# Kernel tuning notes

Measured on AMD Instinct MI355X. Metric: run time of the kernel, lower is better.

Reference implementation:

```python
import jax, jax.numpy as jnp
import numpy as np

B, N, DIN, D, NH, NL = 4, 256, 4, 64, 4, 2
DH = D // NH
EPS = 1e-5
SLOPE = 0.01  # torch LeakyReLU default negative_slope


def setup_inputs() -> dict:
    key = jax.random.key(0)
    ks = jax.random.split(key, 16)
    def p(k, shape, s=0.05):
        return jax.random.normal(k, shape, jnp.float32) * s
    return {
        "feature": jax.random.normal(ks[0], (B, N, N, DIN), jnp.float32),
        "W1": p(ks[1], (DIN, D)), "b1": jnp.zeros((D,), jnp.float32),
        "mw": p(ks[2], (NH, D)), "mb": jnp.zeros((NH,), jnp.float32),
        "bn_gamma": jnp.ones((D,), jnp.float32), "bn_beta": jnp.zeros((D,), jnp.float32),
        "Wq": p(ks[3], (NL, D, D)), "bq": jnp.zeros((NL, D), jnp.float32),
        "Wk": p(ks[4], (NL, D, D)), "bk": jnp.zeros((NL, D), jnp.float32),
        "Wv": p(ks[5], (NL, D, D)), "bv": jnp.zeros((NL, D), jnp.float32),
        "Wo": p(ks[6], (NL, D, D)), "bo": jnp.zeros((NL, D), jnp.float32),
        "ln1_g": jnp.ones((NL, D), jnp.float32), "ln1_b": jnp.zeros((NL, D), jnp.float32),
        "Wff1": p(ks[7], (NL, D, 2 * D)), "bff1": jnp.zeros((NL, 2 * D), jnp.float32),
        "Wff2": p(ks[8], (NL, 2 * D, D)), "bff2": jnp.zeros((NL, D), jnp.float32),
        "ln2_g": jnp.ones((NL, D), jnp.float32), "ln2_b": jnp.zeros((NL, D), jnp.float32),
    }


def _leaky(x):
    return jnp.where(x >= 0, x, SLOPE * x)


def _layer_norm(x, g, b):
    m = x.mean(axis=-1, keepdims=True)
    v = x.var(axis=-1, keepdims=True)
    return g * (x - m) / jnp.sqrt(v + EPS) + b


def reference(feature, W1, b1, mw, mb, bn_gamma, bn_beta,
              Wq, bq, Wk, bk, Wv, bv, Wo, bo, ln1_g, ln1_b,
              Wff1, bff1, Wff2, bff2, ln2_g, ln2_b):
    # linear1: (B,N,N,DIN) -> (B,N,N,D)
    feat = feature @ W1 + b1
    # per-head scalar attention score over node pairs: (NH,B,N,N)
    s = jnp.einsum('bijh,nh->nbij', feat, mw) + mb[:, None, None, None]
    w = jnp.exp(_leaky(s))
    w = w / w.sum(axis=3, keepdims=True)  # softmax-like over second node dim j
    # weighted aggregation: sum over i, then mean over heads -> (B,N,D)
    h = jnp.einsum('nbij,bijh->bjh', w, feat) / NH
    # BatchNorm1d over channels D, stats over (B,N) (training-mode, biased var)
    m = h.mean(axis=(0, 1))
    v = h.var(axis=(0, 1))
    x = bn_gamma * (h - m) / jnp.sqrt(v + EPS) + bn_beta  # (B,N,D)
    # standard post-LN TransformerEncoder, NL layers
    scale = 1.0 / np.sqrt(DH).astype(np.float32)
    for l in range(NL):
        q = (x @ Wq[l] + bq[l]).reshape(B, N, NH, DH)
        k = (x @ Wk[l] + bk[l]).reshape(B, N, NH, DH)
        vv = (x @ Wv[l] + bv[l]).reshape(B, N, NH, DH)
        a = jax.nn.softmax(jnp.einsum('bqhd,bkhd->bhqk', q, k) * scale, axis=-1)
        o = jnp.einsum('bhqk,bkhd->bqhd', a, vv).reshape(B, N, D) @ Wo[l] + bo[l]
        x = _layer_norm(x + o, ln1_g[l], ln1_b[l])
        f = jax.nn.relu(x @ Wff1[l] + bff1[l]) @ Wff2[l] + bff2[l]
        x = _layer_norm(x + f, ln2_g[l], ln2_b[l])
    return x
```

## Files before the change

kernel.cpp:

```cpp
#include <hip/hip_runtime.h>
#include <math.h>

#define B 4
#define N 256
#define DIN 4
#define D 64
#define NH 4
#define NL 2
#define DH 16

constexpr float EPS = 1e-5f;
constexpr float SLOPE = 0.01f;

__device__ __forceinline__ void mc_proj(
    const float* __restrict__ W1, const float* __restrict__ b1,
    const float* __restrict__ mw, const float* __restrict__ mb,
    int lane, float* Mreg , float* Creg ) {
    float w1v[4];
#pragma unroll
    for (int kk = 0; kk < 4; ++kk) w1v[kk] = W1[kk * D + lane];
    float b1v = b1[lane];
#pragma unroll
    for (int n = 0; n < 4; ++n) {
        float mwv = mw[n * D + lane];
        float p0 = w1v[0] * mwv, p1 = w1v[1] * mwv;
        float p2 = w1v[2] * mwv, p3 = w1v[3] * mwv;
        float pc = b1v * mwv;
#pragma unroll
        for (int off = 32; off > 0; off >>= 1) {
            p0 += __shfl_xor(p0, off); p1 += __shfl_xor(p1, off);
            p2 += __shfl_xor(p2, off); p3 += __shfl_xor(p3, off);
            pc += __shfl_xor(pc, off);
        }
        Mreg[n * 4 + 0] = p0; Mreg[n * 4 + 1] = p1;
        Mreg[n * 4 + 2] = p2; Mreg[n * 4 + 3] = p3;
        Creg[n] = pc + mb[n];
    }
}

__global__ void __launch_bounds__(512) k_rowsum(
    const float* __restrict__ feature, const float* __restrict__ W1,
    const float* __restrict__ b1, const float* __restrict__ mw,
    const float* __restrict__ mb, float* __restrict__ rs,
    float* __restrict__ bnacc ) {
    __shared__ float part[32];
    int t = threadIdx.x;
    int lane = t & 63, w = t >> 6;
    int cb = blockIdx.x;
    if (cb == 0 && t < 128) bnacc[t] = 0.f;

    int r = w & 3, mh = w >> 2;
    int bi = cb * 4 + r;
    const float4* fb = (const float4*)(feature) + (size_t)bi * N;
    float4 f0 = fb[lane + 64 * (mh * 2 + 0)];
    float4 f1 = fb[lane + 64 * (mh * 2 + 1)];

    float Mreg[16], Creg[4];
    mc_proj(W1, b1, mw, mb, lane, Mreg, Creg);

    float sn[4] = {0.f, 0.f, 0.f, 0.f};
#pragma unroll
    for (int mm = 0; mm < 2; ++mm) {
        float4 f = (mm == 0) ? f0 : f1;
#pragma unroll
        for (int n = 0; n < 4; ++n) {
            float s = Creg[n] + f.x * Mreg[n*4+0] + f.y * Mreg[n*4+1]
                              + f.z * Mreg[n*4+2] + f.w * Mreg[n*4+3];
            s = (s >= 0.f) ? s : SLOPE * s;
            sn[n] += __expf(s);
        }
    }
#pragma unroll
    for (int n = 0; n < 4; ++n)
#pragma unroll
        for (int off = 32; off > 0; off >>= 1) sn[n] += __shfl_xor(sn[n], off);
    if (lane == 0) {
#pragma unroll
        for (int n = 0; n < 4; ++n) part[w * 4 + n] = sn[n];
    }
    __syncthreads();
    if (t < 16) {
        int rr = t >> 2, n = t & 3;
        rs[((size_t)(cb * 4 + rr)) * 4 + n] = part[rr * 4 + n] + part[(rr + 4) * 4 + n];
    }
}

__global__ void __launch_bounds__(512) k_aggregate(
    const float* __restrict__ feature, const float* __restrict__ W1,
    const float* __restrict__ b1, const float* __restrict__ mw,
    const float* __restrict__ mb, const float* __restrict__ rs,
    float* __restrict__ h, float* __restrict__ bnacc) {
    __shared__ float part[8][10];
    __shared__ float gacc[20];
    __shared__ float hs[4][D];
    int t = threadIdx.x;
    int lane = t & 63, w = t >> 6;
    int cb = blockIdx.x;

    int b = cb >> 6, j0 = (cb & 63) * 4;
    int i = t & 255, jh = t >> 8;
    const float4* fb = (const float4*)(feature) + ((size_t)(b * N + i) * N + j0 + jh * 2);
    float4 f[2];
    f[0] = fb[0];
    f[1] = fb[1];
    float4 r4 = *(const float4*)(rs + (size_t)(b * N + i) * 4);

    float Mreg[16], Creg[4];
    mc_proj(W1, b1, mw, mb, lane, Mreg, Creg);
    float w1v[4];
#pragma unroll
    for (int kk = 0; kk < 4; ++kk) w1v[kk] = W1[kk * D + lane];
    float b1v = b1[lane];

    float rinv[4] = {1.f / r4.x, 1.f / r4.y, 1.f / r4.z, 1.f / r4.w};
    float acc[2][5];
#pragma unroll
    for (int jj = 0; jj < 2; ++jj) {
        float wbar = 0.f;
#pragma unroll
        for (int n = 0; n < 4; ++n) {
            float s = Creg[n] + f[jj].x * Mreg[n*4+0] + f[jj].y * Mreg[n*4+1]
                              + f[jj].z * Mreg[n*4+2] + f[jj].w * Mreg[n*4+3];
            s = (s >= 0.f) ? s : SLOPE * s;
            wbar += __expf(s) * rinv[n];
        }
        wbar *= 0.25f;
        acc[jj][0] = wbar * f[jj].x; acc[jj][1] = wbar * f[jj].y;
        acc[jj][2] = wbar * f[jj].z; acc[jj][3] = wbar * f[jj].w;
        acc[jj][4] = wbar;
    }
#pragma unroll
    for (int jj = 0; jj < 2; ++jj)
#pragma unroll
        for (int c = 0; c < 5; ++c)
#pragma unroll
            for (int off = 32; off > 0; off >>= 1) acc[jj][c] += __shfl_xor(acc[jj][c], off);
    if (lane == 0) {
#pragma unroll
        for (int jj = 0; jj < 2; ++jj)
#pragma unroll
            for (int c = 0; c < 5; ++c) part[w][jj * 5 + c] = acc[jj][c];
    }
    __syncthreads();
    if (t < 20) {
        int jj = t / 5, c = t - jj * 5;
        int g = jj >> 1, jjl = jj & 1;
        gacc[t] = part[g*4+0][jjl*5+c] + part[g*4+1][jjl*5+c]
                + part[g*4+2][jjl*5+c] + part[g*4+3][jjl*5+c];
    }
    __syncthreads();
    if (t < 256) {
        float hv = gacc[w * 5 + 4] * b1v;
#pragma unroll
        for (int kk = 0; kk < 4; ++kk) hv += gacc[w * 5 + kk] * w1v[kk];
        h[((size_t)(b * N + j0 + w)) * D + lane] = hv;
        hs[w][lane] = hv;
    }
    __syncthreads();
    if (t < 64) {
        float s = hs[0][lane] + hs[1][lane] + hs[2][lane] + hs[3][lane];
        float sq = hs[0][lane]*hs[0][lane] + hs[1][lane]*hs[1][lane]
                 + hs[2][lane]*hs[2][lane] + hs[3][lane]*hs[3][lane];
        atomicAdd(bnacc + lane, s);
        atomicAdd(bnacc + D + lane, sq);
    }
}

__global__ void __launch_bounds__(256, 2) k_qkv0(
    const float* __restrict__ h, const float* __restrict__ bnacc,
    const float* __restrict__ bn_g, const float* __restrict__ bn_b,
    const float* __restrict__ Wq, const float* __restrict__ bq,
    const float* __restrict__ Wk, const float* __restrict__ bk,
    const float* __restrict__ Wv, const float* __restrict__ bv,
    float* __restrict__ x, float* __restrict__ q,
    float* __restrict__ k, float* __restrict__ v) {
    __shared__ float xs[2][D];
    __shared__ float pp[4][2][192];
    int t = threadIdx.x, lane = t & 63, w = t >> 6, ch = lane;
    int b = blockIdx.x, n0 = blockIdx.y * 2;

    float wq[16], wk[16], wv[16];
#pragma unroll
    for (int i = 0; i < 16; ++i) {
        int kk = w * 16 + i;
        wq[i] = Wq[kk * D + ch];
        wk[i] = Wk[kk * D + ch];
        wv[i] = Wv[kk * D + ch];
    }
    float mean = bnacc[ch] * (1.0f / (B * N));
    float var = bnacc[D + ch] * (1.0f / (B * N)) - mean * mean;
    float inv = rsqrtf(var + EPS);
    size_t xi0 = ((size_t)(b * N + n0)) * D + ch;
    float xv0 = bn_g[ch] * (h[xi0] - mean) * inv + bn_b[ch];
    float xv1 = bn_g[ch] * (h[xi0 + D] - mean) * inv + bn_b[ch];
    if (w == 0) { x[xi0] = xv0; xs[0][ch] = xv0; }
    if (w == 1) { x[xi0 + D] = xv1; xs[1][ch] = xv1; }
    __syncthreads();

    float aq0=0.f, ak0=0.f, av0=0.f, aq1=0.f, ak1=0.f, av1=0.f;
#pragma unroll
    for (int i = 0; i < 16; ++i) {
        int kk = w * 16 + i;
        float xx0 = xs[0][kk], xx1 = xs[1][kk];
        aq0 += xx0 * wq[i]; ak0 += xx0 * wk[i]; av0 += xx0 * wv[i];
        aq1 += xx1 * wq[i]; ak1 += xx1 * wk[i]; av1 += xx1 * wv[i];
    }
    pp[w][0][ch] = aq0; pp[w][0][64 + ch] = ak0; pp[w][0][128 + ch] = av0;
    pp[w][1][ch] = aq1; pp[w][1][64 + ch] = ak1; pp[w][1][128 + ch] = av1;
    __syncthreads();
    if (w < 3) {
        int o = w * 64;
        int head = ch >> 4, dh = ch & (DH - 1);
#pragma unroll
        for (int tk = 0; tk < 2; ++tk) {
            float val = pp[0][tk][o+ch] + pp[1][tk][o+ch] + pp[2][tk][o+ch] + pp[3][tk][o+ch];
            size_t oidx = (((size_t)(b * NH + head)) * N + (n0 + tk)) * DH + dh;
            if (w == 0) q[oidx] = val + bq[ch];
            else if (w == 1) k[oidx] = val + bk[ch];
            else v[oidx] = val + bv[ch];
        }
    }
}

template <bool FUSE>
__global__ void __launch_bounds__(256, 2) k_layer(
    const float* __restrict__ q, const float* __restrict__ k,
    const float* __restrict__ v,
    const float* __restrict__ Wo, const float* __restrict__ bo,
    const float* __restrict__ ln1g, const float* __restrict__ ln1b,
    const float* __restrict__ Wff1, const float* __restrict__ bff1,
    const float* __restrict__ Wff2, const float* __restrict__ bff2,
    const float* __restrict__ ln2g, const float* __restrict__ ln2b,
    const float* __restrict__ Wqn, const float* __restrict__ bqn,
    const float* __restrict__ Wkn, const float* __restrict__ bkn,
    const float* __restrict__ Wvn, const float* __restrict__ bvn,
    float* __restrict__ qo, float* __restrict__ ko, float* __restrict__ vo,
    float* __restrict__ x) {
    __shared__ float attS[2][D];
    __shared__ float xs[2][D];
    __shared__ float f1s[2][2 * D];
    __shared__ float ppA[4][2][192];
    __shared__ float ppB[4][2][192];
    int t = threadIdx.x, lane = t & 63, w = t >> 6, ch = lane;
    int b = blockIdx.x, n0 = blockIdx.y * 2;

    size_t xi0 = ((size_t)(b * N + n0)) * D + ch;
    float xv0 = x[xi0], xv1 = x[xi0 + D];
    float bo_r = bo[ch], l1g = ln1g[ch], l1b = ln1b[ch];
    float bf1a = bff1[ch], bf1b = bff1[D + ch];
    float bf2_r = bff2[ch], l2g = ln2g[ch], l2b = ln2b[ch];

    int bh = b * NH + w;
    const float4* qp0 = (const float4*)(q + ((size_t)bh * N + n0) * DH);
    const float4* qp1 = (const float4*)(q + ((size_t)bh * N + n0 + 1) * DH);
    float4 qv0[4], qv1[4];
#pragma unroll
    for (int c = 0; c < 4; ++c) { qv0[c] = qp0[c]; qv1[c] = qp1[c]; }
    const float* kb = k + (size_t)bh * N * DH;
    const float* vb = v + (size_t)bh * N * DH;
    float o0[DH], o1[DH];
#pragma unroll
    for (int d = 0; d < DH; ++d) { o0[d] = 0.f; o1[d] = 0.f; }
    float l0 = 0.f, l1 = 0.f;
#pragma unroll 1
    for (int cc = 0; cc < 4; ++cc) {
        int key = cc * 64 + lane;
        const float4* kp4 = (const float4*)(kb + (size_t)key * DH);
        const float4* vp4 = (const float4*)(vb + (size_t)key * DH);
        float4 Kc[4], Vc[4];
#pragma unroll
        for (int c = 0; c < 4; ++c) { Kc[c] = kp4[c]; Vc[c] = vp4[c]; }
        float s0 = 0.f, s1 = 0.f;
#pragma unroll
        for (int c = 0; c < 4; ++c) {
            s0 += qv0[c].x * Kc[c].x + qv0[c].y * Kc[c].y +
                  qv0[c].z * Kc[c].z + qv0[c].w * Kc[c].w;
            s1 += qv1[c].x * Kc[c].x + qv1[c].y * Kc[c].y +
                  qv1[c].z * Kc[c].z + qv1[c].w * Kc[c].w;
        }
        float p0 = __expf(s0 * 0.25f);
        float p1 = __expf(s1 * 0.25f);
        l0 += p0; l1 += p1;
#pragma unroll
        for (int c = 0; c < 4; ++c) {
            o0[4*c+0] += p0 * Vc[c].x; o0[4*c+1] += p0 * Vc[c].y;
            o0[4*c+2] += p0 * Vc[c].z; o0[4*c+3] += p0 * Vc[c].w;
            o1[4*c+0] += p1 * Vc[c].x; o1[4*c+1] += p1 * Vc[c].y;
            o1[4*c+2] += p1 * Vc[c].z; o1[4*c+3] += p1 * Vc[c].w;
        }
    }
    float wo[16];
#pragma unroll
    for (int i = 0; i < 16; ++i) wo[i] = Wo[(w * 16 + i) * D + ch];

#pragma unroll
    for (int off = 32; off > 0; off >>= 1) {
        l0 += __shfl_xor(l0, off);
        l1 += __shfl_xor(l1, off);
    }
#pragma unroll
    for (int d = 0; d < DH; ++d) {
#pragma unroll
        for (int off = 32; off > 0; off >>= 1) {
            o0[d] += __shfl_xor(o0[d], off);
            o1[d] += __shfl_xor(o1[d], off);
        }
    }
    float rl0 = 1.f / l0, rl1 = 1.f / l1;
    if (lane < DH) {
        float sel0 = o0[0], sel1 = o1[0];
#pragma unroll
        for (int d = 1; d < DH; ++d)
            if (lane == d) { sel0 = o0[d]; sel1 = o1[d]; }
        attS[0][w * DH + lane] = sel0 * rl0;
        attS[1][w * DH + lane] = sel1 * rl1;
    }
    __syncthreads();

    {
        float a0 = 0.f, a1 = 0.f;
#pragma unroll
        for (int i = 0; i < 16; ++i) {
            int kk = w * 16 + i;
            float wv = wo[i];
            a0 += attS[0][kk] * wv;
            a1 += attS[1][kk] * wv;
        }
        ppA[w][0][ch] = a0; ppA[w][1][ch] = a1;
    }
    float wf1a[16], wf1b[16];
#pragma unroll
    for (int i = 0; i < 16; ++i) {
        int kk = w * 16 + i;
        wf1a[i] = Wff1[kk * 2 * D + ch];
        wf1b[i] = Wff1[kk * 2 * D + D + ch];
    }
    __syncthreads();

    float r0 = xv0 + bo_r + ppA[0][0][ch] + ppA[1][0][ch] + ppA[2][0][ch] + ppA[3][0][ch];
    float r1 = xv1 + bo_r + ppA[0][1][ch] + ppA[1][1][ch] + ppA[2][1][ch] + ppA[3][1][ch];
    float s0a = r0, q0a = r0 * r0, s1a = r1, q1a = r1 * r1;
#pragma unroll
    for (int off = 32; off > 0; off >>= 1) {
        s0a += __shfl_xor(s0a, off); q0a += __shfl_xor(q0a, off);
        s1a += __shfl_xor(s1a, off); q1a += __shfl_xor(q1a, off);
    }
    float mean10 = s0a * (1.0f / D), var10 = q0a * (1.0f / D) - mean10 * mean10;
    float mean11 = s1a * (1.0f / D), var11 = q1a * (1.0f / D) - mean11 * mean11;
    float x1_0 = l1g * (r0 - mean10) * rsqrtf(var10 + EPS) + l1b;
    float x1_1 = l1g * (r1 - mean11) * rsqrtf(var11 + EPS) + l1b;
    if (w == 0) xs[0][ch] = x1_0;
    if (w == 1) xs[1][ch] = x1_1;
    __syncthreads();

    {
        float u0=0.f, g0=0.f, u1=0.f, g1=0.f;
#pragma unroll
        for (int i = 0; i < 16; ++i) {
            int kk = w * 16 + i;
            float xx0 = xs[0][kk], xx1 = xs[1][kk];
            u0 += xx0 * wf1a[i]; g0 += xx0 * wf1b[i];
            u1 += xx1 * wf1a[i]; g1 += xx1 * wf1b[i];
        }
        ppB[w][0][ch] = u0; ppB[w][0][64 + ch] = g0;
        ppB[w][1][ch] = u1; ppB[w][1][64 + ch] = g1;
    }
    float wf2[32];
#pragma unroll
    for (int i = 0; i < 32; ++i) wf2[i] = Wff2[(w * 32 + i) * D + ch];
    __syncthreads();

    {
        float a00 = fmaxf(bf1a + ppB[0][0][ch] + ppB[1][0][ch] + ppB[2][0][ch] + ppB[3][0][ch], 0.f);
        float a01 = fmaxf(bf1b + ppB[0][0][64+ch] + ppB[1][0][64+ch] + ppB[2][0][64+ch] + ppB[3][0][64+ch], 0.f);
        float a10 = fmaxf(bf1a + ppB[0][1][ch] + ppB[1][1][ch] + ppB[2][1][ch] + ppB[3][1][ch], 0.f);
        float a11 = fmaxf(bf1b + ppB[0][1][64+ch] + ppB[1][1][64+ch] + ppB[2][1][64+ch] + ppB[3][1][64+ch], 0.f);
        if (w == 0) { f1s[0][ch] = a00; f1s[0][64 + ch] = a01; }
        if (w == 1) { f1s[1][ch] = a10; f1s[1][64 + ch] = a11; }
    }
    __syncthreads();

    {
        float e0 = 0.f, e1 = 0.f;
#pragma unroll
        for (int i = 0; i < 32; ++i) {
            int kk = w * 32 + i;
            float xx0 = f1s[0][kk], xx1 = f1s[1][kk];
            e0 += xx0 * wf2[i];
            e1 += xx1 * wf2[i];
        }
        ppA[w][0][ch] = e0; ppA[w][1][ch] = e1;
    }
    float wqn[16], wkn[16], wvn[16];
    if (FUSE) {
#pragma unroll
        for (int i = 0; i < 16; ++i) {
            int kk = w * 16 + i;
            wqn[i] = Wqn[kk * D + ch];
            wkn[i] = Wkn[kk * D + ch];
            wvn[i] = Wvn[kk * D + ch];
        }
    }
    __syncthreads();

    float o2_0 = bf2_r + ppA[0][0][ch] + ppA[1][0][ch] + ppA[2][0][ch] + ppA[3][0][ch];
    float o2_1 = bf2_r + ppA[0][1][ch] + ppA[1][1][ch] + ppA[2][1][ch] + ppA[3][1][ch];
    float r20 = x1_0 + o2_0, r21 = x1_1 + o2_1;
    float s0b = r20, q0b = r20 * r20, s1b = r21, q1b = r21 * r21;
#pragma unroll
    for (int off = 32; off > 0; off >>= 1) {
        s0b += __shfl_xor(s0b, off); q0b += __shfl_xor(q0b, off);
        s1b += __shfl_xor(s1b, off); q1b += __shfl_xor(q1b, off);
    }
    float mean20 = s0b * (1.0f / D), var20 = q0b * (1.0f / D) - mean20 * mean20;
    float mean21 = s1b * (1.0f / D), var21 = q1b * (1.0f / D) - mean21 * mean21;
    float xn0 = l2g * (r20 - mean20) * rsqrtf(var20 + EPS) + l2b;
    float xn1 = l2g * (r21 - mean21) * rsqrtf(var21 + EPS) + l2b;
    if (w == 0) x[xi0] = xn0;
    if (w == 1) x[xi0 + D] = xn1;

    if (FUSE) {
        if (w == 0) xs[0][ch] = xn0;
        if (w == 1) xs[1][ch] = xn1;
        __syncthreads();
        float aq0=0.f, ak0=0.f, av0=0.f, aq1=0.f, ak1=0.f, av1=0.f;
#pragma unroll
        for (int i = 0; i < 16; ++i) {
            int kk = w * 16 + i;
            float xx0 = xs[0][kk], xx1 = xs[1][kk];
            aq0 += xx0 * wqn[i]; ak0 += xx0 * wkn[i]; av0 += xx0 * wvn[i];
            aq1 += xx1 * wqn[i]; ak1 += xx1 * wkn[i]; av1 += xx1 * wvn[i];
        }
        ppB[w][0][ch] = aq0; ppB[w][0][64 + ch] = ak0; ppB[w][0][128 + ch] = av0;
        ppB[w][1][ch] = aq1; ppB[w][1][64 + ch] = ak1; ppB[w][1][128 + ch] = av1;
        __syncthreads();
        if (w < 3) {
            int o = w * 64;
            int head = ch >> 4, dh = ch & (DH - 1);
#pragma unroll
            for (int tk = 0; tk < 2; ++tk) {
                float val = ppB[0][tk][o+ch] + ppB[1][tk][o+ch] + ppB[2][tk][o+ch] + ppB[3][tk][o+ch];
                size_t oidx = (((size_t)(b * NH + head)) * N + (n0 + tk)) * DH + dh;
                if (w == 0) qo[oidx] = val + bqn[ch];
                else if (w == 1) ko[oidx] = val + bkn[ch];
                else vo[oidx] = val + bvn[ch];
            }
        }
    }
}

extern "C" void kernel_launch(void* const* d_in, const int* in_sizes, int n_in,
                              void* d_out, int out_size, void* d_ws, size_t ws_size,
                              hipStream_t stream) {
    const float* feature = (const float*)d_in[0];
    const float* W1   = (const float*)d_in[1];
    const float* b1   = (const float*)d_in[2];
    const float* mw   = (const float*)d_in[3];
    const float* mb   = (const float*)d_in[4];
    const float* bn_g = (const float*)d_in[5];
    const float* bn_b = (const float*)d_in[6];
    const float* Wq   = (const float*)d_in[7];
    const float* bq   = (const float*)d_in[8];
    const float* Wk   = (const float*)d_in[9];
    const float* bk   = (const float*)d_in[10];
    const float* Wv   = (const float*)d_in[11];
    const float* bv   = (const float*)d_in[12];
    const float* Wo   = (const float*)d_in[13];
    const float* bo   = (const float*)d_in[14];
    const float* ln1g = (const float*)d_in[15];
    const float* ln1b = (const float*)d_in[16];
    const float* Wff1 = (const float*)d_in[17];
    const float* bff1 = (const float*)d_in[18];
    const float* Wff2 = (const float*)d_in[19];
    const float* bff2 = (const float*)d_in[20];
    const float* ln2g = (const float*)d_in[21];
    const float* ln2b = (const float*)d_in[22];

    float* ws    = (float*)d_ws;
    float* rs    = ws;
    float* bnacc = rs + B * N * NH;
    float* h     = bnacc + 128;
    float* q     = h + B * N * D;
    float* k0    = q + B * N * D;
    float* v0    = k0 + B * N * D;
    float* k1    = v0 + B * N * D;
    float* v1    = k1 + B * N * D;
    float* x     = (float*)d_out;

    k_rowsum<<<256, 512, 0, stream>>>(feature, W1, b1, mw, mb, rs, bnacc);
    k_aggregate<<<256, 512, 0, stream>>>(feature, W1, b1, mw, mb, rs, h, bnacc);
    k_qkv0<<<dim3(B, N / 2), 256, 0, stream>>>(h, bnacc, bn_g, bn_b,
                                               Wq, bq, Wk, bk, Wv, bv, x, q, k0, v0);
    k_layer<true><<<dim3(B, N / 2), 256, 0, stream>>>(q, k0, v0,
        Wo, bo, ln1g, ln1b, Wff1, bff1, Wff2, bff2, ln2g, ln2b,
        Wq + (size_t)D * D, bq + D, Wk + (size_t)D * D, bk + D,
        Wv + (size_t)D * D, bv + D, q, k1, v1, x);
    k_layer<false><<<dim3(B, N / 2), 256, 0, stream>>>(q, k1, v1,
        Wo + (size_t)D * D, bo + D, ln1g + D, ln1b + D,
        Wff1 + (size_t)D * 2 * D, bff1 + 2 * D,
        Wff2 + (size_t)2 * D * D, bff2 + D, ln2g + D, ln2b + D,
        nullptr, nullptr, nullptr, nullptr, nullptr, nullptr,
        nullptr, nullptr, nullptr, x);
}
```

Before: 147.8 us.

## Fuse row-sum pass into aggregation kernel with per-block recomputation

Merges the row-sum kernel into the aggregation kernel. Each block now recomputes the softmax denominators for every row of its batch into shared memory, replacing the intermediate global buffer and one kernel launch. The accumulator zeroing moves to a hipMemsetAsync. The trade-off is that each of the 64 blocks per batch re-reads that batch's full feature slice and redoes all the exponentials, multiplying that work 64-fold to remove a launch and a global round trip.

Result: slower. 179.8 us (+21.7%).

```diff
diff --git a/kernel.cpp b/kernel.cpp
--- a/kernel.cpp
+++ b/kernel.cpp
@@ -12,14 +12,25 @@
 constexpr float EPS = 1e-5f;
 constexpr float SLOPE = 0.01f;
 
-__device__ __forceinline__ void mc_proj(
-    const float* __restrict__ W1, const float* __restrict__ b1,
-    const float* __restrict__ mw, const float* __restrict__ mb,
-    int lane, float* Mreg , float* Creg ) {
+__global__ void __launch_bounds__(512) k_pre(
+    const float* __restrict__ feature, const float* __restrict__ W1,
+    const float* __restrict__ b1, const float* __restrict__ mw,
+    const float* __restrict__ mb,
+    float* __restrict__ h, float* __restrict__ bnacc) {
+    __shared__ float rsL[N][4];
+    __shared__ float part2[8][10];
+    __shared__ float gacc[20];
+    __shared__ float hs[4][D];
+    int t = threadIdx.x;
+    int lane = t & 63, w = t >> 6;
+    int cb = blockIdx.x;
+    int b = cb >> 6, j0 = (cb & 63) * 4;
+
     float w1v[4];
 #pragma unroll
     for (int kk = 0; kk < 4; ++kk) w1v[kk] = W1[kk * D + lane];
     float b1v = b1[lane];
+    float Mreg[16], Creg[4];
 #pragma unroll
     for (int n = 0; n < 4; ++n) {
         float mwv = mw[n * D + lane];
@@ -36,82 +47,42 @@
         Mreg[n * 4 + 2] = p2; Mreg[n * 4 + 3] = p3;
         Creg[n] = pc + mb[n];
     }
-}
-
-__global__ void __launch_bounds__(512) k_rowsum(
-    const float* __restrict__ feature, const float* __restrict__ W1,
-    const float* __restrict__ b1, const float* __restrict__ mw,
-    const float* __restrict__ mb, float* __restrict__ rs,
-    float* __restrict__ bnacc ) {
-    __shared__ float part[32];
-    int t = threadIdx.x;
-    int lane = t & 63, w = t >> 6;
-    int cb = blockIdx.x;
-    if (cb == 0 && t < 128) bnacc[t] = 0.f;
-
-    int r = w & 3, mh = w >> 2;
-    int bi = cb * 4 + r;
-    const float4* fb = (const float4*)(feature) + (size_t)bi * N;
-    float4 f0 = fb[lane + 64 * (mh * 2 + 0)];
-    float4 f1 = fb[lane + 64 * (mh * 2 + 1)];
-
-    float Mreg[16], Creg[4];
-    mc_proj(W1, b1, mw, mb, lane, Mreg, Creg);
-
-    float sn[4] = {0.f, 0.f, 0.f, 0.f};
-#pragma unroll
-    for (int mm = 0; mm < 2; ++mm) {
-        float4 f = (mm == 0) ? f0 : f1;
-#pragma unroll
-        for (int n = 0; n < 4; ++n) {
-            float s = Creg[n] + f.x * Mreg[n*4+0] + f.y * Mreg[n*4+1]
-                              + f.z * Mreg[n*4+2] + f.w * Mreg[n*4+3];
-            s = (s >= 0.f) ? s : SLOPE * s;
-            sn[n] += __expf(s);
-        }
-    }
-#pragma unroll
-    for (int n = 0; n < 4; ++n)
-#pragma unroll
-        for (int off = 32; off > 0; off >>= 1) sn[n] += __shfl_xor(sn[n], off);
-    if (lane == 0) {
-#pragma unroll
-        for (int n = 0; n < 4; ++n) part[w * 4 + n] = sn[n];
-    }
-    __syncthreads();
-    if (t < 16) {
-        int rr = t >> 2, n = t & 3;
-        rs[((size_t)(cb * 4 + rr)) * 4 + n] = part[rr * 4 + n] + part[(rr + 4) * 4 + n];
-    }
-}
-
-__global__ void __launch_bounds__(512) k_aggregate(
-    const float* __restrict__ feature, const float* __restrict__ W1,
-    const float* __restrict__ b1, const float* __restrict__ mw,
-    const float* __restrict__ mb, const float* __restrict__ rs,
-    float* __restrict__ h, float* __restrict__ bnacc) {
-    __shared__ float part[8][10];
-    __shared__ float gacc[20];
-    __shared__ float hs[4][D];
-    int t = threadIdx.x;
-    int lane = t & 63, w = t >> 6;
-    int cb = blockIdx.x;
-
-    int b = cb >> 6, j0 = (cb & 63) * 4;
+
+    {
+        const float4* fbase = (const float4*)feature + (size_t)b * N * N;
+#pragma unroll 4
+        for (int r = 0; r < 32; ++r) {
+            int i = w + 8 * r;
+            const float4* frow = fbase + (size_t)i * N;
+            float sn[4] = {0.f, 0.f, 0.f, 0.f};
+#pragma unroll
+            for (int m = 0; m < 4; ++m) {
+                float4 f = frow[64 * m + lane];
+#pragma unroll
+                for (int n = 0; n < 4; ++n) {
+                    float s = Creg[n] + f.x * Mreg[n*4+0] + f.y * Mreg[n*4+1]
+                                      + f.z * Mreg[n*4+2] + f.w * Mreg[n*4+3];
+                    s = (s >= 0.f) ? s : SLOPE * s;
+                    sn[n] += __expf(s);
+                }
+            }
+#pragma unroll
+            for (int n = 0; n < 4; ++n)
+#pragma unroll
+                for (int off = 32; off > 0; off >>= 1) sn[n] += __shfl_xor(sn[n], off);
+            if (lane < 4) rsL[i][lane] = (lane == 0) ? sn[0] :
+                                         (lane == 1) ? sn[1] :
+                                         (lane == 2) ? sn[2] : sn[3];
+        }
+    }
+    __syncthreads();
+
     int i = t & 255, jh = t >> 8;
-    const float4* fb = (const float4*)(feature) + ((size_t)(b * N + i) * N + j0 + jh * 2);
+    const float4* fb2 = (const float4*)feature + ((size_t)(b * N + i) * N + j0 + jh * 2);
     float4 f[2];
-    f[0] = fb[0];
-    f[1] = fb[1];
-    float4 r4 = *(const float4*)(rs + (size_t)(b * N + i) * 4);
-
-    float Mreg[16], Creg[4];
-    mc_proj(W1, b1, mw, mb, lane, Mreg, Creg);
-    float w1v[4];
-#pragma unroll
-    for (int kk = 0; kk < 4; ++kk) w1v[kk] = W1[kk * D + lane];
-    float b1v = b1[lane];
-
+    f[0] = fb2[0];
+    f[1] = fb2[1];
+    float4 r4 = *(const float4*)&rsL[i][0];
     float rinv[4] = {1.f / r4.x, 1.f / r4.y, 1.f / r4.z, 1.f / r4.w};
     float acc[2][5];
 #pragma unroll
@@ -139,14 +110,14 @@
 #pragma unroll
         for (int jj = 0; jj < 2; ++jj)
 #pragma unroll
-            for (int c = 0; c < 5; ++c) part[w][jj * 5 + c] = acc[jj][c];
+            for (int c = 0; c < 5; ++c) part2[w][jj * 5 + c] = acc[jj][c];
     }
     __syncthreads();
     if (t < 20) {
         int jj = t / 5, c = t - jj * 5;
         int g = jj >> 1, jjl = jj & 1;
-        gacc[t] = part[g*4+0][jjl*5+c] + part[g*4+1][jjl*5+c]
-                + part[g*4+2][jjl*5+c] + part[g*4+3][jjl*5+c];
+        gacc[t] = part2[g*4+0][jjl*5+c] + part2[g*4+1][jjl*5+c]
+                + part2[g*4+2][jjl*5+c] + part2[g*4+3][jjl*5+c];
     }
     __syncthreads();
     if (t < 256) {
@@ -477,8 +448,7 @@
     const float* ln2b = (const float*)d_in[22];
 
     float* ws    = (float*)d_ws;
-    float* rs    = ws;
-    float* bnacc = rs + B * N * NH;
+    float* bnacc = ws;
     float* h     = bnacc + 128;
     float* q     = h + B * N * D;
     float* k0    = q + B * N * D;
@@ -487,8 +457,8 @@
     float* v1    = k1 + B * N * D;
     float* x     = (float*)d_out;
 
-    k_rowsum<<<256, 512, 0, stream>>>(feature, W1, b1, mw, mb, rs, bnacc);
-    k_aggregate<<<256, 512, 0, stream>>>(feature, W1, b1, mw, mb, rs, h, bnacc);
+    hipMemsetAsync(bnacc, 0, 128 * sizeof(float), stream);
+    k_pre<<<256, 512, 0, stream>>>(feature, W1, b1, mw, mb, h, bnacc);
     k_qkv0<<<dim3(B, N / 2), 256, 0, stream>>>(h, bnacc, bn_g, bn_b,
                                                Wq, bq, Wk, bk, Wv, bv, x, q, k0, v0);
     k_layer<true><<<dim3(B, N / 2), 256, 0, stream>>>(q, k0, v0,
```
